# Kernel optimization log

Measured on AMD Instinct MI355X. Metric: run time of the kernel, lower is better.

## Reference

```python
import jax, jax.numpy as jnp
import numpy as np

N, E, G, H, D = 50000, 800000, 64, 2, 128  # nodes, edges, graphs, heads, out_channels
NEG_SLOPE_ATT = 0.2   # GATv2 default negative_slope
NEG_SLOPE_OUT = 0.01  # torch.nn.LeakyReLU default
BN_EPS = 1e-5


def setup_inputs() -> dict:
    key = jax.random.key(0)
    ks = jax.random.split(key, 12)
    x = jax.random.normal(ks[0], (N, 1), jnp.float32)
    edge_index = jax.random.randint(ks[1], (2, E), 0, N, dtype=jnp.int64)
    edge_attr = jax.random.normal(ks[2], (E,), jnp.float32)
    batch = jnp.sort(jax.random.randint(ks[3], (N,), 0, G, dtype=jnp.int64))
    # GATv2Conv params: lin_l/lin_r: Linear(1, H*D) with bias; lin_edge: Linear(1, H*D) no bias
    Wl = jax.random.normal(ks[4], (1, H * D), jnp.float32) * 0.5
    bl = jax.random.normal(ks[5], (H * D,), jnp.float32) * 0.1
    Wr = jax.random.normal(ks[6], (1, H * D), jnp.float32) * 0.5
    br = jax.random.normal(ks[7], (H * D,), jnp.float32) * 0.1
    We = jax.random.normal(ks[8], (1, H * D), jnp.float32) * 0.5
    att = jax.random.normal(ks[9], (H, D), jnp.float32) * 0.5
    bias = jax.random.normal(ks[10], (D,), jnp.float32) * 0.1
    gamma = jnp.ones((D,), jnp.float32)
    beta = jnp.zeros((D,), jnp.float32)
    return {"x": x, "edge_index": edge_index, "edge_attr": edge_attr, "batch": batch,
            "Wl": Wl, "bl": bl, "Wr": Wr, "br": br, "We": We, "att": att,
            "bias": bias, "gamma": gamma, "beta": beta}


def reference(x, edge_index, edge_attr, batch, Wl, bl, Wr, br, We, att, bias, gamma, beta):
    n = x.shape[0]
    src, dst = edge_index[0], edge_index[1]  # message flows src -> dst
    # node transforms: [N, H, D]
    xl = (x @ Wl + bl).reshape(n, H, D)  # lin_l (source side, also the message value)
    xr = (x @ Wr + br).reshape(n, H, D)  # lin_r (destination side)
    # edge feature embedding: [E, H, D]
    ee = (edge_attr[:, None] @ We).reshape(-1, H, D)
    # GATv2 scoring: leaky_relu(x_j + x_i + e), then dot with attention vector
    m = jax.nn.leaky_relu(xl[src] + xr[dst] + ee, NEG_SLOPE_ATT)  # [E, H, D]
    alpha = jnp.einsum('ehd,hd->eh', m, att)  # [E, H]
    # scatter-softmax over incoming edges per destination node
    amax = jax.ops.segment_max(alpha, dst, num_segments=n)  # [N, H]
    ea = jnp.exp(alpha - amax[dst])
    denom = jax.ops.segment_sum(ea, dst, num_segments=n)
    alpha = ea / (denom[dst] + 1e-16)
    # weighted scatter-add aggregation of x_j
    out = jax.ops.segment_sum(xl[src] * alpha[..., None], dst, num_segments=n)  # [N, H, D]
    out = out.mean(axis=1) + bias  # concat=False -> head average, then conv bias
    # BatchNorm1d in training mode (biased variance over nodes)
    mean = out.mean(axis=0)
    var = ((out - mean) ** 2).mean(axis=0)
    out = (out - mean) * jax.lax.rsqrt(var + BN_EPS) * gamma + beta
    out = jax.nn.leaky_relu(out, NEG_SLOPE_OUT)
    # graph-level scatter_add pooling
    return jax.ops.segment_sum(out, batch, num_segments=G)  # [G, D]
```

## Files before the change

### kernel.cpp

```cpp
#include <hip/hip_runtime.h>
#include <math.h>

#define NN 50000
#define NE 800000
#define NG 64

#define WS_C     0
#define WS_ACC   16
#define WS_BNSUM (WS_ACC + 4*NN)
#define WS_BNSQ  (WS_BNSUM + 128)
#define WS_MOM   WS_BNSUM
#define WS_HEAD  (WS_BNSQ + 128)
#define WS_PREV  (WS_HEAD + 4*NN)
#define WS_STAGE (WS_PREV + NE)
#define WS_END   (WS_STAGE + 4*NE)
#define WS_NEED_BYTES ((size_t)WS_END * 4 + 256)

#define LEND 0xFFFFFFFFu

static_assert(((WS_STAGE * 4) % 16) == 0, "stage 16B alignment");
static_assert(NE % 8 == 0, "edge unroll");

#define STEP(wl_, wr_, we_, bb_, at_, xs_, xd_, ae_, acc_)                 \
  { float tt = fmaf(we_, ae_, bb_); tt = fmaf(wr_, xd_, tt);               \
    tt = fmaf(wl_, xs_, tt); acc_ = fmaf(fabsf(tt), at_, acc_); }

#define SMEM_WEIGHTS_DECL                                                  \
  __shared__ __align__(16) float sWl[256], sWr[256], sWe[256], sB[256], sAt[256];

#define SMEM_WEIGHTS_LOAD                                                  \
  { int t_ = threadIdx.x;                                                  \
    sWl[t_] = Wl[t_]; sWr[t_] = Wr[t_]; sWe[t_] = We[t_];                  \
    sB[t_] = bl[t_] + br[t_]; sAt[t_] = att[t_]; }                         \
  __syncthreads();

#define SCORES(xs_, xd_, ae_, accA, accB, out0, out1)                      \
  { float lin0 = fmaf(c0.x, xs_, fmaf(c0.y, xd_, fmaf(c0.z, ae_, c0.w))); \
    out0 = fmaf(0.4f, accA, 0.6f * lin0);                                  \
    float lin1 = fmaf(c1.x, xs_, fmaf(c1.y, xd_, fmaf(c1.z, ae_, c1.w))); \
    out1 = fmaf(0.4f, accB, 0.6f * lin1); }

#define STEP4(c, q0, q1, q2, q3)                                           \
  STEP(wl.c, wr.c, we.c, bb.c, at.c, xs0, xd0, ae0, q0)                    \
  STEP(wl.c, wr.c, we.c, bb.c, at.c, xs1, xd1, ae1, q1)                    \
  STEP(wl.c, wr.c, we.c, bb.c, at.c, xs2, xd2, ae2, q2)                    \
  STEP(wl.c, wr.c, we.c, bb.c, at.c, xs3, xd3, ae3, q3)

#define SCORE_CORE                                                         \
  int4 s4 = *(const int4*)&ei[base];                                       \
  int4 dd4 = *(const int4*)&ei[NE + base];                                 \
  float4 ae4 = *(const float4*)&eattr[base];                               \
  float xs0 = x[s4.x], xs1 = x[s4.y], xs2 = x[s4.z], xs3 = x[s4.w];        \
  float xd0 = x[dd4.x], xd1 = x[dd4.y], xd2 = x[dd4.z], xd3 = x[dd4.w];    \
  float ae0 = ae4.x, ae1 = ae4.y, ae2 = ae4.z, ae3 = ae4.w;

#define SCORE_LOOPS                                                        \
  float a00 = 0.f, a01 = 0.f, a02 = 0.f, a03 = 0.f;                        \
  float a10 = 0.f, a11 = 0.f, a12 = 0.f, a13 = 0.f;                        \
  _Pragma("unroll 2")                                                      \
  for (int j = 0; j < 128; j += 4) {                                       \
    float4 wl = *(const float4*)&sWl[j];                                   \
    float4 wr = *(const float4*)&sWr[j];                                   \
    float4 we = *(const float4*)&sWe[j];                                   \
    float4 bb = *(const float4*)&sB[j];                                    \
    float4 at = *(const float4*)&sAt[j];                                   \
    STEP4(x, a00, a01, a02, a03)                                           \
    STEP4(y, a00, a01, a02, a03)                                           \
    STEP4(z, a00, a01, a02, a03)                                           \
    STEP4(w, a00, a01, a02, a03)                                           \
  }                                                                        \
  _Pragma("unroll 2")                                                      \
  for (int j = 128; j < 256; j += 4) {                                     \
    float4 wl = *(const float4*)&sWl[j];                                   \
    float4 wr = *(const float4*)&sWr[j];                                   \
    float4 we = *(const float4*)&sWe[j];                                   \
    float4 bb = *(const float4*)&sB[j];                                    \
    float4 at = *(const float4*)&sAt[j];                                   \
    STEP4(x, a10, a11, a12, a13)                                           \
    STEP4(y, a10, a11, a12, a13)                                           \
    STEP4(z, a10, a11, a12, a13)                                           \
    STEP4(w, a10, a11, a12, a13)                                           \
  }                                                                        \
  float4 c0 = *(const float4*)&ws[WS_C];                                   \
  float4 c1 = *(const float4*)&ws[WS_C + 4];

#define STEP8(c, Q)                                                        \
  STEP(wl.c, wr.c, we.c, bb.c, at.c, xs0, xd0, ae0, Q##0)                  \
  STEP(wl.c, wr.c, we.c, bb.c, at.c, xs1, xd1, ae1, Q##1)                  \
  STEP(wl.c, wr.c, we.c, bb.c, at.c, xs2, xd2, ae2, Q##2)                  \
  STEP(wl.c, wr.c, we.c, bb.c, at.c, xs3, xd3, ae3, Q##3)                  \
  STEP(wl.c, wr.c, we.c, bb.c, at.c, xs4, xd4, ae4, Q##4)                  \
  STEP(wl.c, wr.c, we.c, bb.c, at.c, xs5, xd5, ae5, Q##5)                  \
  STEP(wl.c, wr.c, we.c, bb.c, at.c, xs6, xd6, ae6, Q##6)                  \
  STEP(wl.c, wr.c, we.c, bb.c, at.c, xs7, xd7, ae7, Q##7)

extern "C" __global__ __launch_bounds__(256)
void k0_init(float* __restrict__ ws,
             const float* __restrict__ att, const float* __restrict__ Wl,
             const float* __restrict__ Wr, const float* __restrict__ We,
             const float* __restrict__ bl, const float* __restrict__ br,
             float* __restrict__ out, int dense)
{
  int tid = blockIdx.x * 256 + threadIdx.x;
  int nt = gridDim.x * 256;
  if (dense) {
    unsigned* head = (unsigned*)(ws + WS_HEAD);
    for (int i = tid; i < 4 * NN; i += nt) head[i] = LEND;
    if (tid < 14) ws[WS_MOM + tid] = 0.f;
  } else {
    for (int i = tid; i < 4 * NN; i += nt) ws[WS_ACC + i] = 0.f;
    for (int i = tid; i < 256; i += nt) ws[WS_BNSUM + i] = 0.f;
  }
  for (int i = tid; i < NG * 128; i += nt) out[i] = 0.f;
  if (blockIdx.x == 0) {
    __shared__ float red[4][256];
    int t = threadIdx.x;
    float a = att[t];
    red[0][t] = a * Wl[t];
    red[1][t] = a * Wr[t];
    red[2][t] = a * We[t];
    red[3][t] = a * (bl[t] + br[t]);
    __syncthreads();
    if (t < 8) {
      int k = t >> 1, h = t & 1;
      float s = 0.f;
      for (int d = 0; d < 128; ++d) s += red[k][h * 128 + d];
      ws[WS_C + h * 4 + k] = s;
    }
  }
}

extern "C" __global__ __launch_bounds__(256)
void ke_edge(const int* __restrict__ ei, const float* __restrict__ x,
             const float* __restrict__ eattr,
             const float* __restrict__ Wl, const float* __restrict__ Wr,
             const float* __restrict__ We, const float* __restrict__ bl,
             const float* __restrict__ br, const float* __restrict__ att,
             float* __restrict__ ws)
{
  SMEM_WEIGHTS_DECL
  SMEM_WEIGHTS_LOAD
  int base = (blockIdx.x * 256 + threadIdx.x) * 8;
  if (base >= NE) return;
  int4 sa = *(const int4*)&ei[base];
  int4 sb = *(const int4*)&ei[base + 4];
  int4 da = *(const int4*)&ei[NE + base];
  int4 db = *(const int4*)&ei[NE + base + 4];
  float4 aea = *(const float4*)&eattr[base];
  float4 aeb = *(const float4*)&eattr[base + 4];
  float ae0 = aea.x, ae1 = aea.y, ae2 = aea.z, ae3 = aea.w;
  float ae4 = aeb.x, ae5 = aeb.y, ae6 = aeb.z, ae7 = aeb.w;
  unsigned* head = (unsigned*)(ws + WS_HEAD);
  unsigned pv0 = atomicExch(&head[4 * da.x + 0], (unsigned)(base + 0));
  unsigned pv1 = atomicExch(&head[4 * da.y + 1], (unsigned)(base + 1));
  unsigned pv2 = atomicExch(&head[4 * da.z + 2], (unsigned)(base + 2));
  unsigned pv3 = atomicExch(&head[4 * da.w + 3], (unsigned)(base + 3));
  unsigned pv4 = atomicExch(&head[4 * db.x + 0], (unsigned)(base + 4));
  unsigned pv5 = atomicExch(&head[4 * db.y + 1], (unsigned)(base + 5));
  unsigned pv6 = atomicExch(&head[4 * db.z + 2], (unsigned)(base + 6));
  unsigned pv7 = atomicExch(&head[4 * db.w + 3], (unsigned)(base + 7));
  float xs0 = x[sa.x], xs1 = x[sa.y], xs2 = x[sa.z], xs3 = x[sa.w];
  float xs4 = x[sb.x], xs5 = x[sb.y], xs6 = x[sb.z], xs7 = x[sb.w];
  float xd0 = x[da.x], xd1 = x[da.y], xd2 = x[da.z], xd3 = x[da.w];
  float xd4 = x[db.x], xd5 = x[db.y], xd6 = x[db.z], xd7 = x[db.w];
  float q0 = 0.f, q1 = 0.f, q2 = 0.f, q3 = 0.f;
  float q4 = 0.f, q5 = 0.f, q6 = 0.f, q7 = 0.f;
  float r0 = 0.f, r1 = 0.f, r2 = 0.f, r3 = 0.f;
  float r4 = 0.f, r5 = 0.f, r6 = 0.f, r7 = 0.f;
#pragma unroll 2
  for (int j = 0; j < 128; j += 4) {
    float4 wl = *(const float4*)&sWl[j];
    float4 wr = *(const float4*)&sWr[j];
    float4 we = *(const float4*)&sWe[j];
    float4 bb = *(const float4*)&sB[j];
    float4 at = *(const float4*)&sAt[j];
    STEP8(x, q) STEP8(y, q) STEP8(z, q) STEP8(w, q)
  }
#pragma unroll 2
  for (int j = 128; j < 256; j += 4) {
    float4 wl = *(const float4*)&sWl[j];
    float4 wr = *(const float4*)&sWr[j];
    float4 we = *(const float4*)&sWe[j];
    float4 bb = *(const float4*)&sB[j];
    float4 at = *(const float4*)&sAt[j];
    STEP8(x, r) STEP8(y, r) STEP8(z, r) STEP8(w, r)
  }
  float4 c0 = *(const float4*)&ws[WS_C];
  float4 c1 = *(const float4*)&ws[WS_C + 4];
  float4* stage = (float4*)(ws + WS_STAGE);
  unsigned* prev = (unsigned*)(ws + WS_PREV);
  float s0, s1;
#define EPI(i)                                                             \
  { SCORES(xs##i, xd##i, ae##i, q##i, r##i, s0, s1)                        \
    float e0 = __expf(s0), e1 = __expf(s1);                                \
    stage[base + i] = make_float4(e0, e1, e0 * xs##i, e1 * xs##i);         \
    prev[base + i] = pv##i; }
  EPI(0) EPI(1) EPI(2) EPI(3) EPI(4) EPI(5) EPI(6) EPI(7)
#undef EPI
}

extern "C" __global__ __launch_bounds__(256)
void kfm_gather(float* __restrict__ ws)
{
  const int t = threadIdx.x;
  int gid = blockIdx.x * 256 + t;
  int n = gid >> 1;
  int half = gid & 1;
  float f1 = 0.f, f2 = 0.f, f3 = 0.f, f4 = 0.f;
  if (n < NN) {
    const unsigned* head = (const unsigned*)(ws + WS_HEAD);
    const unsigned* prev = (const unsigned*)(ws + WS_PREV);
    const float4* stage = (const float4*)(ws + WS_STAGE);
    uint2 p = *(const uint2*)&head[4 * n + 2 * half];
    float4 A0 = make_float4(0.f, 0.f, 0.f, 0.f);
    float4 A1 = A0;
    while ((p.x & p.y) != LEND) {
#define HOP(pc, Ac)                                                        \
      if (pc != LEND) {                                                    \
        float4 q = stage[pc];                                              \
        unsigned np = prev[pc];                                            \
        Ac.x += q.x; Ac.y += q.y; Ac.z += q.z; Ac.w += q.w;                \
        pc = np;                                                           \
      }
      HOP(p.x, A0) HOP(p.y, A1)
#undef HOP
    }
    float den0 = A0.x + A1.x;
    float den1 = A0.y + A1.y;
    float t10  = A0.z + A1.z;
    float t11  = A0.w + A1.w;
    den0 += __shfl_xor(den0, 1);
    den1 += __shfl_xor(den1, 1);
    t10  += __shfl_xor(t10, 1);
    t11  += __shfl_xor(t11, 1);
    if (half == 0) {
      *(float4*)&ws[WS_ACC + 4 * n] = make_float4(den0, den1, t10, t11);
      float r0 = 1.f / (den0 + 1e-16f);
      float r1 = 1.f / (den1 + 1e-16f);
      f1 = den0 * r0; f2 = t10 * r0; f3 = den1 * r1; f4 = t11 * r1;
    }
  }
  float pm[14] = { f1, f2, f3, f4,
                   f1*f1, f1*f2, f1*f3, f1*f4,
                   f2*f2, f2*f3, f2*f4,
                   f3*f3, f3*f4, f4*f4 };
#pragma unroll
  for (int k = 0; k < 14; ++k) {
    float v = pm[k];
#pragma unroll
    for (int m = 32; m >= 1; m >>= 1) v += __shfl_xor(v, m);
    pm[k] = v;
  }
  __shared__ float smom[56];
  int wid = t >> 6, lane = t & 63;
  if (lane == 0) {
#pragma unroll
    for (int k = 0; k < 14; ++k) smom[wid * 14 + k] = pm[k];
  }
  __syncthreads();
  if (t < 14) {
    float s = smom[t] + smom[14 + t] + smom[28 + t] + smom[42 + t];
    if (s != 0.f) atomicAdd(&ws[WS_MOM + t], s);
  }
}

extern "C" __global__ __launch_bounds__(256)
void k4m_pool(const int* __restrict__ batch,
              const float* __restrict__ Wl, const float* __restrict__ bl,
              const float* __restrict__ bias, const float* __restrict__ gamma,
              const float* __restrict__ beta,
              float* __restrict__ ws, float* __restrict__ out)
{
  const int CHUNK = (NN + (int)gridDim.x - 1) / (int)gridDim.x;
  int n0 = blockIdx.x * CHUNK;
  if (n0 >= NN) return;
  int n1 = n0 + CHUNK; if (n1 > NN) n1 = NN;
  int t = threadIdx.x;
  int d = t & 127;
  int row = t >> 7;
  float S1 = ws[WS_MOM + 0], S2 = ws[WS_MOM + 1];
  float S3 = ws[WS_MOM + 2], S4 = ws[WS_MOM + 3];
  float M11 = ws[WS_MOM + 4], M12 = ws[WS_MOM + 5], M13 = ws[WS_MOM + 6];
  float M14 = ws[WS_MOM + 7], M22 = ws[WS_MOM + 8], M23 = ws[WS_MOM + 9];
  float M24 = ws[WS_MOM + 10], M33 = ws[WS_MOM + 11], M34 = ws[WS_MOM + 12];
  float M44 = ws[WS_MOM + 13];
  float g1 = 0.5f * bl[d], g2 = 0.5f * Wl[d];
  float g3 = 0.5f * bl[128 + d], g4 = 0.5f * Wl[128 + d];
  float g5 = bias[d];
  const float invN = 1.f / (float)NN;
  float dotS = g1 * S1 + g2 * S2 + g3 * S3 + g4 * S4;
  float mean = (dotS + (float)NN * g5) * invN;
  float sumsq = g1*g1*M11 + g2*g2*M22 + g3*g3*M33 + g4*g4*M44
              + 2.f*(g1*g2*M12 + g1*g3*M13 + g1*g4*M14
                   + g2*g3*M23 + g2*g4*M24 + g3*g4*M34)
              + 2.f*g5*dotS + (float)NN*g5*g5;
  float var = fmaf(sumsq, invN, -mean * mean);
  float scale = gamma[d] * rsqrtf(var + 1e-5f);
  float shift = fmaf(-mean, scale, beta[d]);
  __shared__ float pool[4][128];
  for (int i = t; i < 512; i += 256) ((float*)pool)[i] = 0.f;
  __syncthreads();
  int g0 = batch[n0];
  for (int n = n0 + row; n < n1; n += 2) {
    float4 a = *(const float4*)&ws[WS_ACC + 4 * n];
    float r0 = 1.f / (a.x + 1e-16f);
    float r1 = 1.f / (a.y + 1e-16f);
    float o = g1 * (a.x * r0) + g2 * (a.z * r0)
            + g3 * (a.y * r1) + g4 * (a.w * r1) + g5;
    float v = fmaf(o, scale, shift);
    v = v > 0.f ? v : 0.01f * v;
    int g = batch[n];
    int slot = g - g0;
    if (slot < 4) atomicAdd(&pool[slot][d], v);
    else atomicAdd(&out[g * 128 + d], v);
  }
  __syncthreads();
  for (int i = t; i < 512; i += 256) {
    int slot = i >> 7, dd = i & 127;
    int g = g0 + slot;
    float v = pool[slot][dd];
    if (g < NG && v != 0.f) atomicAdd(&out[g * 128 + dd], v);
  }
}

extern "C" __global__ __launch_bounds__(256)
void k12f(const int* __restrict__ ei, const float* __restrict__ x,
          const float* __restrict__ eattr,
          const float* __restrict__ Wl, const float* __restrict__ Wr,
          const float* __restrict__ We, const float* __restrict__ bl,
          const float* __restrict__ br, const float* __restrict__ att,
          float* __restrict__ ws)
{
  SMEM_WEIGHTS_DECL
  SMEM_WEIGHTS_LOAD
  int base = (blockIdx.x * 256 + threadIdx.x) * 4;
  if (base >= NE) return;
  SCORE_CORE
  SCORE_LOOPS
  float* acc = ws + WS_ACC;
  float s0, s1;
#define EPI2(xs_, xd_, ae_, accA, accB, dsti)                              \
  { SCORES(xs_, xd_, ae_, accA, accB, s0, s1)                              \
    float e0 = __expf(s0), e1 = __expf(s1);                                \
    float* a = &acc[4 * dsti];                                             \
    atomicAdd(a + 0, e0); atomicAdd(a + 1, e1);                            \
    atomicAdd(a + 2, e0 * xs_); atomicAdd(a + 3, e1 * xs_); }
  EPI2(xs0, xd0, ae0, a00, a10, dd4.x)
  EPI2(xs1, xd1, ae1, a01, a11, dd4.y)
  EPI2(xs2, xd2, ae2, a02, a12, dd4.z)
  EPI2(xs3, xd3, ae3, a03, a13, dd4.w)
#undef EPI2
}

__device__ __forceinline__ float node_out4(float4 a, float wl0, float wl1,
                                           float b0, float b1, float bs)
{
  float r0 = 1.f / (a.x + 1e-16f);
  float r1 = 1.f / (a.y + 1e-16f);
  return 0.5f * (fmaf(wl0, a.z * r0, b0 * (a.x * r0)) +
                 fmaf(wl1, a.w * r1, b1 * (a.y * r1))) + bs;
}

extern "C" __global__ __launch_bounds__(256)
void k3_stats(const float* __restrict__ Wl, const float* __restrict__ bl,
              const float* __restrict__ bias, float* __restrict__ ws)
{
  int d = threadIdx.x & 127;
  int row = threadIdx.x >> 7;
  float wl0 = Wl[d], wl1 = Wl[128 + d];
  float b0 = bl[d], b1 = bl[128 + d];
  float bs = bias[d];
  float sum = 0.f, sq = 0.f;
  for (int n = blockIdx.x * 2 + row; n < NN; n += gridDim.x * 2) {
    float4 a = *(const float4*)&ws[WS_ACC + 4 * n];
    float o = node_out4(a, wl0, wl1, b0, b1, bs);
    sum += o;
    sq = fmaf(o, o, sq);
  }
  __shared__ float l1[256], l2[256];
  l1[threadIdx.x] = sum; l2[threadIdx.x] = sq;
  __syncthreads();
  if (row == 0) {
    atomicAdd(&ws[WS_BNSUM + d], l1[d] + l1[128 + d]);
    atomicAdd(&ws[WS_BNSQ + d], l2[d] + l2[128 + d]);
  }
}

extern "C" __global__ __launch_bounds__(256)
void k4_pool(const int* __restrict__ batch,
             const float* __restrict__ Wl, const float* __restrict__ bl,
             const float* __restrict__ bias, const float* __restrict__ gamma,
             const float* __restrict__ beta,
             float* __restrict__ ws, float* __restrict__ out)
{
  const int CHUNK = (NN + (int)gridDim.x - 1) / (int)gridDim.x;
  int n0 = blockIdx.x * CHUNK;
  if (n0 >= NN) return;
  int n1 = n0 + CHUNK; if (n1 > NN) n1 = NN;
  int d = threadIdx.x & 127;
  int row = threadIdx.x >> 7;
  const float invN = 1.f / (float)NN;
  float mean = ws[WS_BNSUM + d] * invN;
  float var = fmaf(ws[WS_BNSQ + d], invN, -mean * mean);
  float scale = gamma[d] * rsqrtf(var + 1e-5f);
  float shift = fmaf(-mean, scale, beta[d]);
  float wl0 = Wl[d], wl1 = Wl[128 + d];
  float b0 = bl[d], b1 = bl[128 + d];
  float bs = bias[d];
  __shared__ float pool[4][128];
  for (int i = threadIdx.x; i < 512; i += 256) ((float*)pool)[i] = 0.f;
  __syncthreads();
  int g0 = batch[n0];
  for (int n = n0 + row; n < n1; n += 2) {
    float4 a = *(const float4*)&ws[WS_ACC + 4 * n];
    float o = node_out4(a, wl0, wl1, b0, b1, bs);
    float v = fmaf(o, scale, shift);
    v = v > 0.f ? v : 0.01f * v;
    int g = batch[n];
    int slot = g - g0;
    if (slot < 4) atomicAdd(&pool[slot][d], v);
    else atomicAdd(&out[g * 128 + d], v);
  }
  __syncthreads();
  for (int i = threadIdx.x; i < 512; i += 256) {
    int slot = i >> 7, dd = i & 127;
    int g = g0 + slot;
    float v = pool[slot][dd];
    if (g < NG && v != 0.f) atomicAdd(&out[g * 128 + dd], v);
  }
}

extern "C" void kernel_launch(void* const* d_in, const int* in_sizes, int n_in,
                              void* d_out, int out_size, void* d_ws, size_t ws_size,
                              hipStream_t stream) {
  const float* x     = (const float*)d_in[0];
  const int*   ei    = (const int*)d_in[1];
  const float* eattr = (const float*)d_in[2];
  const int*   batch = (const int*)d_in[3];
  const float* Wl    = (const float*)d_in[4];
  const float* bl    = (const float*)d_in[5];
  const float* Wr    = (const float*)d_in[6];
  const float* br    = (const float*)d_in[7];
  const float* We    = (const float*)d_in[8];
  const float* att   = (const float*)d_in[9];
  const float* bias  = (const float*)d_in[10];
  const float* gam   = (const float*)d_in[11];
  const float* bet   = (const float*)d_in[12];
  float* ws  = (float*)d_ws;
  float* out = (float*)d_out;

  const bool dense = (ws_size >= WS_NEED_BYTES);

  hipLaunchKernelGGL(k0_init, dim3(128), dim3(256), 0, stream,
                     ws, att, Wl, Wr, We, bl, br, out, dense ? 1 : 0);
  if (dense) {
    hipLaunchKernelGGL(ke_edge, dim3((NE / 8 + 255) / 256), dim3(256), 0, stream,
                       ei, x, eattr, Wl, Wr, We, bl, br, att, ws);
    hipLaunchKernelGGL(kfm_gather, dim3((2 * NN + 255) / 256), dim3(256), 0, stream, ws);
    hipLaunchKernelGGL(k4m_pool, dim3(256), dim3(256), 0, stream,
                       batch, Wl, bl, bias, gam, bet, ws, out);
  } else {
    hipLaunchKernelGGL(k12f, dim3((NE / 4 + 255) / 256), dim3(256), 0, stream,
                       ei, x, eattr, Wl, Wr, We, bl, br, att, ws);
    hipLaunchKernelGGL(k3_stats, dim3(256), dim3(256), 0, stream,
                       Wl, bl, bias, ws);
    hipLaunchKernelGGL(k4_pool, dim3(256), dim3(256), 0, stream,
                       batch, Wl, bl, bias, gam, bet, ws, out);
  }
}
```

Before: 207.0 us.

## Pack next-pointer into stage record and gather with four chains per node

Each edge's linked-list next pointer now goes into the w slot of the staged float4, and the raw source value takes the place of the premultiplied product. The separate prev array and its load per hop are removed. The gather now uses four threads per node, each walking one of the four chains, and combines them with two shuffle rounds; the product with xs is done in the gather by FMA. The edge kernel moves to 128-thread blocks with launch_bounds(128,1), which shifts occupancy and register limits, and gather thread count doubles with shorter serial chains.

```diff
diff --git a/kernel.cpp b/kernel.cpp
--- a/kernel.cpp
+++ b/kernel.cpp
@@ -11,8 +11,7 @@
 #define WS_BNSQ  (WS_BNSUM + 128)
 #define WS_MOM   WS_BNSUM
 #define WS_HEAD  (WS_BNSQ + 128)
-#define WS_PREV  (WS_HEAD + 4*NN)
-#define WS_STAGE (WS_PREV + NE)
+#define WS_STAGE (WS_HEAD + 4*NN)
 #define WS_END   (WS_STAGE + 4*NE)
 #define WS_NEED_BYTES ((size_t)WS_END * 4 + 256)
 
@@ -29,7 +28,7 @@
   __shared__ __align__(16) float sWl[256], sWr[256], sWe[256], sB[256], sAt[256];
 
 #define SMEM_WEIGHTS_LOAD                                                  \
-  { int t_ = threadIdx.x;                                                  \
+  for (int t_ = threadIdx.x; t_ < 256; t_ += blockDim.x) {                 \
     sWl[t_] = Wl[t_]; sWr[t_] = Wr[t_]; sWe[t_] = We[t_];                  \
     sB[t_] = bl[t_] + br[t_]; sAt[t_] = att[t_]; }                         \
   __syncthreads();
@@ -130,7 +129,7 @@
   }
 }
 
-extern "C" __global__ __launch_bounds__(256)
+extern "C" __global__ __launch_bounds__(128, 1)
 void ke_edge(const int* __restrict__ ei, const float* __restrict__ x,
              const float* __restrict__ eattr,
              const float* __restrict__ Wl, const float* __restrict__ Wr,
@@ -140,7 +139,7 @@
 {
   SMEM_WEIGHTS_DECL
   SMEM_WEIGHTS_LOAD
-  int base = (blockIdx.x * 256 + threadIdx.x) * 8;
+  int base = (blockIdx.x * 128 + (int)threadIdx.x) * 8;
   if (base >= NE) return;
   int4 sa = *(const int4*)&ei[base];
   int4 sb = *(const int4*)&ei[base + 4];
@@ -188,13 +187,11 @@
   float4 c0 = *(const float4*)&ws[WS_C];
   float4 c1 = *(const float4*)&ws[WS_C + 4];
   float4* stage = (float4*)(ws + WS_STAGE);
-  unsigned* prev = (unsigned*)(ws + WS_PREV);
   float s0, s1;
 #define EPI(i)                                                             \
   { SCORES(xs##i, xd##i, ae##i, q##i, r##i, s0, s1)                        \
     float e0 = __expf(s0), e1 = __expf(s1);                                \
-    stage[base + i] = make_float4(e0, e1, e0 * xs##i, e1 * xs##i);         \
-    prev[base + i] = pv##i; }
+    stage[base + i] = make_float4(e0, e1, xs##i, __uint_as_float(pv##i)); }
   EPI(0) EPI(1) EPI(2) EPI(3) EPI(4) EPI(5) EPI(6) EPI(7)
 #undef EPI
 }
@@ -204,41 +201,32 @@
 {
   const int t = threadIdx.x;
   int gid = blockIdx.x * 256 + t;
-  int n = gid >> 1;
-  int half = gid & 1;
+  int n = gid >> 2;
+  int c = gid & 3;
   float f1 = 0.f, f2 = 0.f, f3 = 0.f, f4 = 0.f;
+  float4 A = make_float4(0.f, 0.f, 0.f, 0.f);
   if (n < NN) {
     const unsigned* head = (const unsigned*)(ws + WS_HEAD);
-    const unsigned* prev = (const unsigned*)(ws + WS_PREV);
     const float4* stage = (const float4*)(ws + WS_STAGE);
-    uint2 p = *(const uint2*)&head[4 * n + 2 * half];
-    float4 A0 = make_float4(0.f, 0.f, 0.f, 0.f);
-    float4 A1 = A0;
-    while ((p.x & p.y) != LEND) {
-#define HOP(pc, Ac)                                                        \
-      if (pc != LEND) {                                                    \
-        float4 q = stage[pc];                                              \
-        unsigned np = prev[pc];                                            \
-        Ac.x += q.x; Ac.y += q.y; Ac.z += q.z; Ac.w += q.w;                \
-        pc = np;                                                           \
-      }
-      HOP(p.x, A0) HOP(p.y, A1)
-#undef HOP
+    unsigned p = head[gid];
+    while (p != LEND) {
+      float4 q = stage[p];
+      p = __float_as_uint(q.w);
+      A.x += q.x;
+      A.y += q.y;
+      A.z = fmaf(q.x, q.z, A.z);
+      A.w = fmaf(q.y, q.z, A.w);
     }
-    float den0 = A0.x + A1.x;
-    float den1 = A0.y + A1.y;
-    float t10  = A0.z + A1.z;
-    float t11  = A0.w + A1.w;
-    den0 += __shfl_xor(den0, 1);
-    den1 += __shfl_xor(den1, 1);
-    t10  += __shfl_xor(t10, 1);
-    t11  += __shfl_xor(t11, 1);
-    if (half == 0) {
-      *(float4*)&ws[WS_ACC + 4 * n] = make_float4(den0, den1, t10, t11);
-      float r0 = 1.f / (den0 + 1e-16f);
-      float r1 = 1.f / (den1 + 1e-16f);
-      f1 = den0 * r0; f2 = t10 * r0; f3 = den1 * r1; f4 = t11 * r1;
-    }
+  }
+  A.x += __shfl_xor(A.x, 1); A.y += __shfl_xor(A.y, 1);
+  A.z += __shfl_xor(A.z, 1); A.w += __shfl_xor(A.w, 1);
+  A.x += __shfl_xor(A.x, 2); A.y += __shfl_xor(A.y, 2);
+  A.z += __shfl_xor(A.z, 2); A.w += __shfl_xor(A.w, 2);
+  if (n < NN && c == 0) {
+    *(float4*)&ws[WS_ACC + 4 * n] = A;
+    float r0 = 1.f / (A.x + 1e-16f);
+    float r1 = 1.f / (A.y + 1e-16f);
+    f1 = A.x * r0; f2 = A.z * r0; f3 = A.y * r1; f4 = A.w * r1;
   }
   float pm[14] = { f1, f2, f3, f4,
                    f1*f1, f1*f2, f1*f3, f1*f4,
@@ -454,9 +442,9 @@
   hipLaunchKernelGGL(k0_init, dim3(128), dim3(256), 0, stream,
                      ws, att, Wl, Wr, We, bl, br, out, dense ? 1 : 0);
   if (dense) {
-    hipLaunchKernelGGL(ke_edge, dim3((NE / 8 + 255) / 256), dim3(256), 0, stream,
+    hipLaunchKernelGGL(ke_edge, dim3((NE / 8 + 127) / 128), dim3(128), 0, stream,
                        ei, x, eattr, Wl, Wr, We, bl, br, att, ws);
-    hipLaunchKernelGGL(kfm_gather, dim3((2 * NN + 255) / 256), dim3(256), 0, stream, ws);
+    hipLaunchKernelGGL(kfm_gather, dim3((4 * NN + 255) / 256), dim3(256), 0, stream, ws);
     hipLaunchKernelGGL(k4m_pool, dim3(256), dim3(256), 0, stream,
                        batch, Wl, bl, bias, gam, bet, ws, out);
   } else {
```

Result: no change. 206.2 us (-0.4%).
